# Performance work log

Measured on AMD Instinct MI355X. Metric: run time of the kernel, lower is better.

## Reference

```python
import jax, jax.numpy as jnp
import numpy as np


def setup_inputs() -> dict:
    key = jax.random.key(0)
    ks = jax.random.split(key, 7)
    B, C, N, F = 4, 8, 2048, 64
    H, O = 64, 64
    s_in = 1.0 / np.sqrt(F)
    s_h = 1.0 / np.sqrt(H)
    return {
        "x": jax.random.normal(ks[0], (B, C, N, F), dtype=jnp.float32),
        "W1": jax.random.uniform(ks[1], (H, F), jnp.float32, -s_in, s_in),
        "b1": jax.random.uniform(ks[2], (H,), jnp.float32, -s_in, s_in),
        "W2": jax.random.uniform(ks[3], (H, F), jnp.float32, -s_in, s_in),
        "b2": jax.random.uniform(ks[4], (H,), jnp.float32, -s_in, s_in),
        "W3": jax.random.uniform(ks[5], (O, F), jnp.float32, -s_in, s_in),
        "b3": jax.random.uniform(ks[6], (O,), jnp.float32, -s_in, s_in),
    }


def reference(x, W1, b1, W2, b2, W3, b3):
    # e1, e2: [B,C,N,H]  (torch Linear: x @ W^T + b)
    e1 = jnp.einsum("bcnf,hf->bcnh", x, W1) + b1
    e2 = jnp.einsum("bcnf,hf->bcnh", x, W2) + b2
    # adjacency via ReLU(e1 @ e2^T): [B,C,N,N]
    adj = jax.nn.relu(jnp.einsum("bcnh,bcmh->bcnm", e1, e2))
    # propagate: [B,C,N,F]
    h = jnp.einsum("bcnm,bcmf->bcnf", adj, x)
    # output projection (linear3): [B,C,N,O]
    return jnp.einsum("bcnf,of->bcno", h, W3) + b3
```

## Files before the change

kernel.cpp:

```cpp
#include <hip/hip_runtime.h>
#include <hip/hip_bf16.h>

#define BCH 32
#define NN  2048
#define DD  64

typedef __attribute__((ext_vector_type(8)))  __bf16 bf16x8;
typedef __attribute__((ext_vector_type(4)))  __bf16 bf16x4;
typedef __attribute__((ext_vector_type(4)))  float  f32x4;
typedef __attribute__((ext_vector_type(16))) float  f32x16;
typedef __attribute__((ext_vector_type(2)))  int    i32x2;
typedef __attribute__((ext_vector_type(4)))  int    i32x4;
typedef __attribute__((ext_vector_type(2)))  unsigned int u32x2;

__device__ inline f32x4 mfma16(bf16x8 a, bf16x8 b, f32x4 c) {
    return __builtin_amdgcn_mfma_f32_16x16x32_bf16(a, b, c, 0, 0, 0);
}
__device__ inline f32x16 mfma32(bf16x8 a, bf16x8 b, f32x16 c) {
    return __builtin_amdgcn_mfma_f32_32x32x16_bf16(a, b, c, 0, 0, 0);
}
__device__ inline void plswap(int& a, int& b) {
    u32x2 r = __builtin_amdgcn_permlane32_swap((unsigned)a, (unsigned)b, false, false);
    a = (int)r[0];
    b = (int)r[1];
}

__global__ __launch_bounds__(256) void prep_kernel(
    const float* __restrict__ x,
    const float* __restrict__ W1, const float* __restrict__ b1,
    const float* __restrict__ W2, const float* __restrict__ b2,
    const float* __restrict__ W3,
    __bf16* __restrict__ e1f, __bf16* __restrict__ e2f, __bf16* __restrict__ vtf)
{
    const int t   = threadIdx.x;
    const int blk = blockIdx.x;
    const int bc  = blk >> 5, st = blk & 31;
    const long grow = (long)bc * NN + st * 64;
    const int w = t >> 6, l = t & 63, lg = l >> 4, li = l & 15;

    bf16x8 a[4][2];
    #pragma unroll
    for (int nb = 0; nb < 4; ++nb)
        #pragma unroll
        for (int kk = 0; kk < 2; ++kk) {
            const float* p = x + (grow + nb * 16 + li) * DD + kk * 32 + lg * 8;
            f32x4 v0 = *(const f32x4*)p, v1 = *(const f32x4*)(p + 4);
            #pragma unroll
            for (int j = 0; j < 4; ++j) {
                a[nb][kk][j]     = (__bf16)v0[j];
                a[nb][kk][4 + j] = (__bf16)v1[j];
            }
        }

    bf16x8 wf1[2], wf2[2], wf3[2];
    #pragma unroll
    for (int kk = 0; kk < 2; ++kk) {
        const float* p1 = W1 + (w * 16 + li) * DD + kk * 32 + lg * 8;
        const float* p2 = W2 + (w * 16 + li) * DD + kk * 32 + lg * 8;
        const float* p3 = W3 + (w * 16 + li) * DD + kk * 32 + lg * 8;
        f32x4 u0 = *(const f32x4*)p1, u1 = *(const f32x4*)(p1 + 4);
        f32x4 v0 = *(const f32x4*)p2, v1 = *(const f32x4*)(p2 + 4);
        f32x4 t0 = *(const f32x4*)p3, t1 = *(const f32x4*)(p3 + 4);
        #pragma unroll
        for (int j = 0; j < 4; ++j) {
            wf1[kk][j] = (__bf16)u0[j]; wf1[kk][4 + j] = (__bf16)u1[j];
            wf2[kk][j] = (__bf16)v0[j]; wf2[kk][4 + j] = (__bf16)v1[j];
            wf3[kk][j] = (__bf16)t0[j]; wf3[kk][4 + j] = (__bf16)t1[j];
        }
    }
    const f32x4 bq1 = *(const f32x4*)(b1 + w * 16 + lg * 4);
    const f32x4 bq2 = *(const f32x4*)(b2 + w * 16 + lg * 4);

    const size_t tbase = (size_t)(bc * 32 + st) * 4096;

    #pragma unroll
    for (int nb = 0; nb < 4; ++nb) {
        f32x4 acc1 = {0.f,0.f,0.f,0.f}, acc2 = {0.f,0.f,0.f,0.f}, acc3 = {0.f,0.f,0.f,0.f};
        #pragma unroll
        for (int kk = 0; kk < 2; ++kk) {
            acc1 = mfma16(wf1[kk], a[nb][kk], acc1);
            acc2 = mfma16(wf2[kk], a[nb][kk], acc2);
            acc3 = mfma16(a[nb][kk], wf3[kk], acc3);
        }
        bf16x4 q1, q2, q3;
        #pragma unroll
        for (int r = 0; r < 4; ++r) {
            q1[r] = (__bf16)(acc1[r] + bq1[r]);
            q2[r] = (__bf16)(acc2[r] + bq2[r]);
            q3[r] = (__bf16)acc3[r];
        }
        *(bf16x4*)&e1f[tbase + (w * 2 + (lg >> 1)) * 512 + (nb * 16 + li) * 8 + (lg & 1) * 4] = q1;
        *(bf16x4*)&e2f[tbase + (w * 2 + (lg >> 1)) * 512 + (nb * 16 + li) * 8 + (lg & 1) * 4] = q2;
        *(bf16x4*)&vtf[tbase + (nb * 2 + (lg >> 1)) * 512 + (w * 16 + li) * 8 + (lg & 1) * 4] = q3;
    }
}

__global__ __launch_bounds__(128, 2) void fused_kernel(
    const __bf16* __restrict__ e1f, const __bf16* __restrict__ e2f,
    const __bf16* __restrict__ vtf, const float* __restrict__ b3,
    float* __restrict__ out)
{
    __shared__ float scratch[4096];

    const int t   = threadIdx.x;
    const int bid = blockIdx.x;
    const int x8 = bid & 7, jj = bid >> 3;
    const int bc = x8 * 4 + (jj >> 5), nt = jj & 31;

    const int wm = t >> 6, l = t & 63;
    const int l31 = l & 31, hi5 = l >> 5;
    const int nbase = nt * 64;

    const float bv0 = b3[l31], bv1 = b3[32 + l31];

    bf16x8 e1v[2][4];
    #pragma unroll
    for (int nb = 0; nb < 2; ++nb) {
        const __bf16* p = e1f + ((size_t)bc * 32 + nt) * 4096 + hi5 * 512 + (nb * 32 + l31) * 8;
        #pragma unroll
        for (int kk = 0; kk < 4; ++kk)
            e1v[nb][kk] = *(const bf16x8*)(p + kk * 1024);
    }

    f32x16 fz;
    #pragma unroll
    for (int i = 0; i < 16; ++i) fz[i] = 0.f;
    f32x16 hacc[2][2];
    #pragma unroll
    for (int nb = 0; nb < 2; ++nb)
        #pragma unroll
        for (int fb = 0; fb < 2; ++fb)
            #pragma unroll
            for (int i = 0; i < 16; ++i) hacc[nb][fb][i] = 0.f;

    const __bf16* E2 = e2f + (size_t)bc * 131072 + hi5 * 512 + (wm * 32 + l31) * 8;
    const __bf16* VT = vtf + (size_t)bc * 131072 + (wm * 4 + hi5) * 512 + l31 * 8;

    auto loadEF = [&](int kt, bf16x8 (&ef)[4]) {
        const __bf16* p = E2 + (size_t)kt * 4096;
        #pragma unroll
        for (int kk = 0; kk < 4; ++kk)
            ef[kk] = *(const bf16x8*)(p + kk * 1024);
    };
    auto loadVF = [&](int kt, bf16x8 (&vf)[4]) {
        const __bf16* p = VT + (size_t)kt * 4096;
        #pragma unroll
        for (int kk2 = 0; kk2 < 2; ++kk2) {
            vf[kk2 * 2 + 0] = *(const bf16x8*)(p + kk2 * 1024);
            vf[kk2 * 2 + 1] = *(const bf16x8*)(p + kk2 * 1024 + 256);
        }
    };
    auto computeS = [&](bf16x8 (&ef)[4], f32x16 (&sT)[2]) {
        sT[0] = mfma32(ef[0], e1v[0][0], fz);
        sT[1] = mfma32(ef[0], e1v[1][0], fz);
        #pragma unroll
        for (int kk = 1; kk < 4; ++kk) {
            sT[0] = mfma32(ef[kk], e1v[0][kk], sT[0]);
            sT[1] = mfma32(ef[kk], e1v[1][kk], sT[1]);
        }
    };
    auto packQ = [&](const f32x16 (&sT)[2], i32x2 (&Q)[2][4]) {
        #pragma unroll
        for (int nb = 0; nb < 2; ++nb)
            #pragma unroll
            for (int g = 0; g < 4; ++g) {
                bf16x4 q0;
                #pragma unroll
                for (int r = 0; r < 4; ++r)
                    q0[r] = (__bf16)fmaxf(sT[nb][4 * g + r], 0.f);
                Q[nb][g] = __builtin_bit_cast(i32x2, q0);
            }
    };
    auto doPV = [&](i32x2 (&Q)[2][4], bf16x8 (&vf)[4]) {
        #pragma unroll
        for (int kk2 = 0; kk2 < 2; ++kk2)
            #pragma unroll
            for (int nb = 0; nb < 2; ++nb) {
                int a0 = Q[nb][2 * kk2][0],     a1 = Q[nb][2 * kk2][1];
                int b0 = Q[nb][2 * kk2 + 1][0], b1 = Q[nb][2 * kk2 + 1][1];
                plswap(a0, b0);
                plswap(a1, b1);
                i32x4 pfi = { a0, a1, b0, b1 };
                bf16x8 pf = __builtin_bit_cast(bf16x8, pfi);
                hacc[nb][0] = mfma32(pf, vf[kk2 * 2 + 0], hacc[nb][0]);
                hacc[nb][1] = mfma32(pf, vf[kk2 * 2 + 1], hacc[nb][1]);
            }
    };

    bf16x8 efA[4], vfA[4], efB[4], vfB[4];
    i32x2 Qa[2][4], Qb[2][4];
    f32x16 sT[2];

    loadEF(0, efA); loadVF(0, vfA);
    for (int kt = 0; kt < 32; kt += 2) {
        loadEF(kt + 1, efB); loadVF(kt + 1, vfB);
        computeS(efA, sT);
        packQ(sT, Qa);
        doPV(Qa, vfA);
        if (kt + 2 < 32) { loadEF(kt + 2, efA); loadVF(kt + 2, vfA); }
        computeS(efB, sT);
        packQ(sT, Qb);
        doPV(Qb, vfB);
    }

    if (wm == 1) {
        #pragma unroll
        for (int nb = 0; nb < 2; ++nb)
            #pragma unroll
            for (int q = 0; q < 8; ++q) {
                f32x4 v;
                #pragma unroll
                for (int r = 0; r < 4; ++r) {
                    const int idx = q * 4 + r;
                    v[r] = hacc[nb][idx >> 4][idx & 15];
                }
                *(f32x4*)&scratch[nb * 2048 + q * 256 + l * 4] = v;
            }
    }
    __syncthreads();
    if (wm == 0) {
        #pragma unroll
        for (int nb = 0; nb < 2; ++nb)
            #pragma unroll
            for (int q = 0; q < 8; ++q) {
                f32x4 v = *(const f32x4*)&scratch[nb * 2048 + q * 256 + l * 4];
                #pragma unroll
                for (int r = 0; r < 4; ++r) {
                    const int idx = q * 4 + r;
                    hacc[nb][idx >> 4][idx & 15] += v[r];
                }
            }
        #pragma unroll
        for (int nb = 0; nb < 2; ++nb) {
            const size_t ob = ((size_t)bc * NN + nbase + nb * 32) * DD;
            #pragma unroll
            for (int reg = 0; reg < 16; ++reg) {
                const int n = (reg & 3) + 8 * (reg >> 2) + 4 * hi5;
                out[ob + (size_t)n * DD + l31]      = hacc[nb][0][reg] + bv0;
                out[ob + (size_t)n * DD + 32 + l31] = hacc[nb][1][reg] + bv1;
            }
        }
    }
}

extern "C" void kernel_launch(void* const* d_in, const int* in_sizes, int n_in,
                              void* d_out, int out_size, void* d_ws, size_t ws_size,
                              hipStream_t stream) {
    const float* x  = (const float*)d_in[0];
    const float* W1 = (const float*)d_in[1];
    const float* b1 = (const float*)d_in[2];
    const float* W2 = (const float*)d_in[3];
    const float* b2 = (const float*)d_in[4];
    const float* W3 = (const float*)d_in[5];
    const float* b3 = (const float*)d_in[6];
    float* out = (float*)d_out;

    __bf16* e1f = (__bf16*)d_ws;
    __bf16* e2f = e1f + (size_t)BCH * NN * DD;
    __bf16* vtf = e2f + (size_t)BCH * NN * DD;

    prep_kernel<<<dim3(1024), dim3(256), 0, stream>>>(x, W1, b1, W2, b2, W3, e1f, e2f, vtf);
    fused_kernel<<<dim3(1024), dim3(128), 0, stream>>>(e1f, e2f, vtf, b3, out);
}
```

Measured before the change: 59.86 us.

## Split key loop across four waves with two-stage LDS reduction

```diff
diff --git a/kernel.cpp b/kernel.cpp
--- a/kernel.cpp
+++ b/kernel.cpp
@@ -95,19 +95,20 @@
     }
 }
 
-__global__ __launch_bounds__(128, 2) void fused_kernel(
+__global__ __launch_bounds__(256, 3) void fused_kernel(
     const __bf16* __restrict__ e1f, const __bf16* __restrict__ e2f,
     const __bf16* __restrict__ vtf, const float* __restrict__ b3,
     float* __restrict__ out)
 {
-    __shared__ float scratch[4096];
+    __shared__ float scratch[8192];
 
     const int t   = threadIdx.x;
     const int bid = blockIdx.x;
     const int x8 = bid & 7, jj = bid >> 3;
     const int bc = x8 * 4 + (jj >> 5), nt = jj & 31;
 
-    const int wm = t >> 6, l = t & 63;
+    const int w = t >> 6, l = t & 63;
+    const int wm = w & 1, kp = w >> 1;
     const int l31 = l & 31, hi5 = l >> 5;
     const int nbase = nt * 64;
 
@@ -191,19 +192,23 @@
     i32x2 Qa[2][4], Qb[2][4];
     f32x16 sT[2];
 
-    loadEF(0, efA); loadVF(0, vfA);
-    for (int kt = 0; kt < 32; kt += 2) {
-        loadEF(kt + 1, efB); loadVF(kt + 1, vfB);
+    loadEF(kp, efA); loadVF(kp, vfA);
+    for (int j = 0; j < 16; j += 2) {
+        const int ktB = 2 * (j + 1) + kp;
+        loadEF(ktB, efB); loadVF(ktB, vfB);
         computeS(efA, sT);
         packQ(sT, Qa);
         doPV(Qa, vfA);
-        if (kt + 2 < 32) { loadEF(kt + 2, efA); loadVF(kt + 2, vfA); }
+        if (j + 2 < 16) {
+            const int ktA = 2 * (j + 2) + kp;
+            loadEF(ktA, efA); loadVF(ktA, vfA);
+        }
         computeS(efB, sT);
         packQ(sT, Qb);
         doPV(Qb, vfB);
     }
 
-    if (wm == 1) {
+    if (kp == 1) {
         #pragma unroll
         for (int nb = 0; nb < 2; ++nb)
             #pragma unroll
@@ -214,11 +219,40 @@
                     const int idx = q * 4 + r;
                     v[r] = hacc[nb][idx >> 4][idx & 15];
                 }
+                *(f32x4*)&scratch[wm * 4096 + nb * 2048 + q * 256 + l * 4] = v;
+            }
+    }
+    __syncthreads();
+    if (kp == 0) {
+        #pragma unroll
+        for (int nb = 0; nb < 2; ++nb)
+            #pragma unroll
+            for (int q = 0; q < 8; ++q) {
+                f32x4 v = *(const f32x4*)&scratch[wm * 4096 + nb * 2048 + q * 256 + l * 4];
+                #pragma unroll
+                for (int r = 0; r < 4; ++r) {
+                    const int idx = q * 4 + r;
+                    hacc[nb][idx >> 4][idx & 15] += v[r];
+                }
+            }
+    }
+    __syncthreads();
+    if (kp == 0 && wm == 1) {
+        #pragma unroll
+        for (int nb = 0; nb < 2; ++nb)
+            #pragma unroll
+            for (int q = 0; q < 8; ++q) {
+                f32x4 v;
+                #pragma unroll
+                for (int r = 0; r < 4; ++r) {
+                    const int idx = q * 4 + r;
+                    v[r] = hacc[nb][idx >> 4][idx & 15];
+                }
                 *(f32x4*)&scratch[nb * 2048 + q * 256 + l * 4] = v;
             }
     }
     __syncthreads();
-    if (wm == 0) {
+    if (kp == 0 && wm == 0) {
         #pragma unroll
         for (int nb = 0; nb < 2; ++nb)
             #pragma unroll
@@ -260,5 +294,5 @@
     __bf16* vtf = e2f + (size_t)BCH * NN * DD;
 
     prep_kernel<<<dim3(1024), dim3(256), 0, stream>>>(x, W1, b1, W2, b2, W3, e1f, e2f, vtf);
-    fused_kernel<<<dim3(1024), dim3(128), 0, stream>>>(e1f, e2f, vtf, b3, out);
-}
+    fused_kernel<<<dim3(1024), dim3(256), 0, stream>>>(e1f, e2f, vtf, b3, out);
+}
```

After: 108.5 us. +81.3%, slower.
